# Kernel optimization log

Hardware: AMD Instinct MI355X
Metric: run time of the kernel (lower is better)

Reference implementation:

```python
import jax, jax.numpy as jnp
import numpy as np

N_NODES = 10000
W_DIM = 512
N_EDGES = 200000


def setup_inputs() -> dict:
    key = jax.random.key(0)
    k1, k2, k3 = jax.random.split(key, 3)
    z_drug = jax.random.normal(k1, (N_NODES, W_DIM), dtype=jnp.float32)
    # glorot-style init for the bilinear weight
    glorot_std = jnp.sqrt(2.0 / (W_DIM + W_DIM)).astype(jnp.float32)
    weight = jax.random.normal(k2, (W_DIM, W_DIM), dtype=jnp.float32) * glorot_std
    batch_edges = jax.random.randint(k3, (2, N_EDGES), 0, N_NODES, dtype=jnp.int64)
    return {"z_drug": z_drug, "weight": weight, "batch_edges": batch_edges}


def reference(z_drug, weight, batch_edges):
    # edge_type == 'drug_drug': both endpoints come from the drug table.
    row_embed = z_drug[batch_edges[0]]  # [E, d]
    col_embed = z_drug[batch_edges[1]]  # [E, d]
    # score_e = row_e @ W @ col_e  == diag((Z1 W) Z2^T) without the N x N blowup
    score = jnp.einsum('ed,df,ef->e', row_embed, weight, col_embed)
    return jax.nn.sigmoid(score)  # is_sigmoid=True default
```

## Files before the change

### kernel.cpp

```cpp
#include <hip/hip_runtime.h>
#include <math.h>

#define DIM     512
#define NNODES  10000
#define NEDGES  200000
#define MPAD    10048
#define NMB     157
#define NGRP    5
#define NB      (NGRP * NNODES)
#define SCAN_N  49
#define GEMM_GRID (NMB * 4)

#define HIST_BLK   50
#define SCAN_BASE  50
#define SCAT_BASE  99
#define SCAT_N     98
#define GEMM_BASE  197
#define FUSE_GRID  (GEMM_BASE + GEMM_GRID)

using floatx4 = __attribute__((ext_vector_type(4))) float;
using half8   = __attribute__((ext_vector_type(8))) _Float16;
using half2v  = __attribute__((ext_vector_type(2))) _Float16;

__device__ inline float dot2acc(half2v a, half2v b, float c) {
#if __has_builtin(__builtin_amdgcn_fdot2)
    return __builtin_amdgcn_fdot2(a, b, c, false);
#else
    return fmaf((float)a[0], (float)b[0], fmaf((float)a[1], (float)b[1], c));
#endif
}

__device__ inline int aload(const int* p) {
    return __hip_atomic_load(p, __ATOMIC_RELAXED, __HIP_MEMORY_SCOPE_AGENT);
}
__device__ inline void astore(int* p, int v) {
    __hip_atomic_store(p, v, __ATOMIC_RELAXED, __HIP_MEMORY_SCOPE_AGENT);
}
__device__ inline void waitflag(int* f, int target) {
    while (__hip_atomic_load(f, __ATOMIC_RELAXED, __HIP_MEMORY_SCOPE_AGENT) < target)
        __builtin_amdgcn_s_sleep(8);
    __atomic_signal_fence(__ATOMIC_ACQUIRE);
}
__device__ inline void signal(int* f) {
    __atomic_signal_fence(__ATOMIC_RELEASE);
    __hip_atomic_fetch_add(f, 1, __ATOMIC_RELAXED, __HIP_MEMORY_SCOPE_AGENT);
}

#define PREP_ZBLK 2512
__global__ __launch_bounds__(256) void prep(const float* __restrict__ Z,
                                            const float* __restrict__ W,
                                            _Float16* __restrict__ Zh16,
                                            _Float16* __restrict__ Wh16t,
                                            int* __restrict__ counts,
                                            int* __restrict__ flags) {
    const int b = blockIdx.x;
    const int t = threadIdx.x;

    if (b == 0 && t < 4) flags[t] = 0;

    if (b < 196) {
        int i = b * 256 + t;
        if (i < NB) counts[i] = 0;
    }

    if (b < PREP_ZBLK) {
        const int idx8 = (b * 256 + t) * 8;
        const int m = idx8 >> 9;
        float x[8];
        if (m < NNODES) {
            float4 v0 = *(const float4*)(Z + idx8);
            float4 v1 = *(const float4*)(Z + idx8 + 4);
            x[0]=v0.x; x[1]=v0.y; x[2]=v0.z; x[3]=v0.w;
            x[4]=v1.x; x[5]=v1.y; x[6]=v1.z; x[7]=v1.w;
        } else {
            #pragma unroll
            for (int j = 0; j < 8; ++j) x[j] = 0.f;
        }
        half8 h;
        #pragma unroll
        for (int j = 0; j < 8; ++j) h[j] = (_Float16)x[j];
        *(half8*)(Zh16 + idx8) = h;
    } else {
        __shared__ float tile[64][65];
        const int wb = b - PREP_ZBLK;
        const int kb = (wb >> 3) * 64;
        const int nb = (wb & 7) * 64;
        const int kk = t >> 2;
        const int ch = t & 3;

        const float* src = W + (size_t)(kb + kk) * DIM + nb + ch * 16;
        #pragma unroll
        for (int q = 0; q < 4; ++q) {
            float4 v = *(const float4*)(src + q * 4);
            tile[kk][ch * 16 + q * 4 + 0] = v.x;
            tile[kk][ch * 16 + q * 4 + 1] = v.y;
            tile[kk][ch * 16 + q * 4 + 2] = v.z;
            tile[kk][ch * 16 + q * 4 + 3] = v.w;
        }
        __syncthreads();

        const int nn = kk;
        half8 h0, h1;
        #pragma unroll
        for (int i = 0; i < 8; ++i) h0[i] = (_Float16)tile[ch * 16 + i][nn];
        #pragma unroll
        for (int i = 0; i < 8; ++i) h1[i] = (_Float16)tile[ch * 16 + 8 + i][nn];
        _Float16* d = Wh16t + (size_t)(nb + nn) * DIM + kb + ch * 16;
        *(half8*)(d)     = h0;
        *(half8*)(d + 8) = h1;
    }
}

__global__ __launch_bounds__(256, 3) void gemm_sort(
        const _Float16* __restrict__ Zh16,
        const _Float16* __restrict__ Wh16t,
        _Float16* __restrict__ ZWh,
        const int* __restrict__ eidx,
        int* __restrict__ counts,
        int* __restrict__ cursor,
        int* __restrict__ blksum,
        unsigned* __restrict__ keys,
        unsigned short* __restrict__ rows16,
        int* __restrict__ flags)
{
    __shared__ _Float16 Abuf[2][2 * 64 * 32];
    __shared__ _Float16 Bbuf[2][2 * 128 * 32];
    __shared__ int wsum[4];
    __shared__ int sbase;

    const int t   = threadIdx.x;
    const int bid = blockIdx.x;

    if (bid >= GEMM_BASE) {
        const int vb    = bid - GEMM_BASE;
        const int n_idx = vb & 3;
        const int m0    = (vb >> 2) * 64;
        const int n0    = n_idx * 128;

        const int l  = t & 63;
        const int w  = t >> 6;
        const int wn = w * 32;
        const int lm = l & 15;
        const int lq = l >> 4;
        const unsigned wbase = (unsigned)(t & 192);

        floatx4 acc[4][2] = {};

        auto stage = [&](int buf, int k0) {
            #pragma unroll
            for (int p = 0; p < 2; ++p) {
                const int s   = p * 256 + t;
                const int kk  = s >> 8;
                const int row = (s >> 2) & 63;
                const int ch  = s & 3;
                const _Float16* src = Zh16 + (size_t)(m0 + row) * DIM + k0 + kk * 32 + ch * 8;
                __builtin_amdgcn_global_load_lds(
                    (const __attribute__((address_space(1))) void*)src,
                    (__attribute__((address_space(3))) void*)&Abuf[buf][(p * 256 + wbase) * 8],
                    16, 0, 0);
            }
            #pragma unroll
            for (int p = 0; p < 4; ++p) {
                const int s   = p * 256 + t;
                const int kk  = s >> 9;
                const int row = (s >> 2) & 127;
                const int ch  = s & 3;
                const _Float16* src = Wh16t + (size_t)(n0 + row) * DIM + k0 + kk * 32 + ch * 8;
                __builtin_amdgcn_global_load_lds(
                    (const __attribute__((address_space(1))) void*)src,
                    (__attribute__((address_space(3))) void*)&Bbuf[buf][(p * 256 + wbase) * 8],
                    16, 0, 0);
            }
        };

        stage(0, 0);
        __syncthreads();

        for (int s = 0; s < 8; ++s) {
            const int buf = s & 1;
            if (s < 7) stage(buf ^ 1, (s + 1) * 64);

            #pragma unroll
            for (int kk = 0; kk < 2; ++kk) {
                half8 aF[4], bF[2];
                #pragma unroll
                for (int i = 0; i < 4; ++i)
                    aF[i] = *(const half8*)&Abuf[buf][kk * 2048 + (16 * i + lm) * 32 + lq * 8];
                #pragma unroll
                for (int j = 0; j < 2; ++j)
                    bF[j] = *(const half8*)&Bbuf[buf][kk * 4096 + (wn + 16 * j + lm) * 32 + lq * 8];

                #pragma unroll
                for (int i = 0; i < 4; ++i)
                    #pragma unroll
                    for (int j = 0; j < 2; ++j)
                        acc[i][j] = __builtin_amdgcn_mfma_f32_16x16x32_f16(aF[i], bF[j], acc[i][j], 0, 0, 0);
            }
            __syncthreads();
        }

        #pragma unroll
        for (int i = 0; i < 4; ++i)
            #pragma unroll
            for (int j = 0; j < 2; ++j)
                #pragma unroll
                for (int r = 0; r < 4; ++r) {
                    const int gm = m0 + 16 * i + lq * 4 + r;
                    const int gn = n0 + wn + 16 * j + lm;
                    if (gm < NNODES)
                        ZWh[(size_t)gm * DIM + gn] = (_Float16)acc[i][j][r];
                }
        return;
    }

    if (bid < HIST_BLK) {
        for (int e = bid * 256 + t; e < NEDGES; e += HIST_BLK * 256) {
            int r = eidx[e];
            int c = eidx[NEDGES + e];
            atomicAdd(&counts[(c >> 11) * NNODES + r], 1);
        }
        __syncthreads();
        if (t == 0) signal(&flags[0]);
        return;
    }

    if (bid < SCAT_BASE) {
        const int b = bid - SCAN_BASE;
        const int lane = t & 63;
        const int wv   = t >> 6;

        if (t == 0) waitflag(&flags[0], HIST_BLK);
        __syncthreads();

        const int base = b * 1024 + t * 4;
        int v0 = 0, v1 = 0, v2 = 0, v3 = 0;
        if (base + 3 < NB) {
            v0 = aload(counts + base);
            v1 = aload(counts + base + 1);
            v2 = aload(counts + base + 2);
            v3 = aload(counts + base + 3);
        } else {
            if (base     < NB) v0 = aload(counts + base);
            if (base + 1 < NB) v1 = aload(counts + base + 1);
            if (base + 2 < NB) v2 = aload(counts + base + 2);
        }
        const int ts = v0 + v1 + v2 + v3;
        int incl = ts;
        #pragma unroll
        for (int off = 1; off < 64; off <<= 1) {
            int u = __shfl_up(incl, off, 64);
            if (lane >= off) incl += u;
        }
        if (lane == 63) wsum[wv] = incl;
        __syncthreads();
        int wb = 0;
        #pragma unroll
        for (int k = 0; k < 4; ++k) if (k < wv) wb += wsum[k];
        const int ex   = wb + incl - ts;
        const int pre0 = ex;
        const int pre1 = ex + v0;
        const int pre2 = pre1 + v1;
        const int pre3 = pre2 + v2;
        if (t == 255) astore(blksum + b, wb + incl);
        __syncthreads();
        if (t == 0) { signal(&flags[1]); waitflag(&flags[1], SCAN_N); }
        __syncthreads();

        if (t < 64) {
            int v = (t < b) ? aload(blksum + t) : 0;
            #pragma unroll
            for (int off = 32; off > 0; off >>= 1)
                v += __shfl_xor(v, off, 64);
            if (t == 0) sbase = v;
        }
        __syncthreads();
        const int b0 = sbase;

        if (base + 3 < NB) {
            astore(cursor + base,     b0 + pre0);
            astore(cursor + base + 1, b0 + pre1);
            astore(cursor + base + 2, b0 + pre2);
            astore(cursor + base + 3, b0 + pre3);
        } else {
            if (base     < NB) astore(cursor + base,     b0 + pre0);
            if (base + 1 < NB) astore(cursor + base + 1, b0 + pre1);
            if (base + 2 < NB) astore(cursor + base + 2, b0 + pre2);
        }
        __syncthreads();
        if (t == 0) signal(&flags[2]);
        return;
    }

    {
        if (t == 0) waitflag(&flags[2], SCAN_N);
        __syncthreads();

        for (int e = (bid - SCAT_BASE) * 256 + t; e < NEDGES; e += SCAT_N * 256) {
            int r = eidx[e];
            int c = eidx[NEDGES + e];
            int pos = atomicAdd(&cursor[(c >> 11) * NNODES + r], 1);
            keys[pos]   = ((unsigned)c << 18) | (unsigned)e;
            rows16[pos] = (unsigned short)r;
        }
    }
}

__global__ __launch_bounds__(256) void edge_score_f(const _Float16* __restrict__ ZWh,
                                                    const _Float16* __restrict__ Zh,
                                                    const unsigned* __restrict__ keys,
                                                    const unsigned short* __restrict__ rows16,
                                                    float* __restrict__ out) {
    const int t    = threadIdx.x;
    const int wgid = blockIdx.x * 4 + (t >> 6);
    const int lane = t & 63;
    const int gq   = lane >> 4;
    const int sl   = lane & 15;

    const int ii = wgid * 4 + gq;
    const unsigned k = keys[ii];
    const int c = (int)(k >> 18);
    const int r = (int)rows16[ii];

    const _Float16* rp = ZWh + (size_t)r * DIM + sl * 32;
    const _Float16* cp = Zh  + (size_t)c * DIM + sl * 32;

    half8 ra0 = *(const half8*)(rp);
    half8 ra1 = *(const half8*)(rp + 8);
    half8 ra2 = *(const half8*)(rp + 16);
    half8 ra3 = *(const half8*)(rp + 24);
    half8 c0  = *(const half8*)(cp);
    half8 c1  = *(const half8*)(cp + 8);
    half8 c2  = *(const half8*)(cp + 16);
    half8 c3  = *(const half8*)(cp + 24);

    float s = 0.f;
    #pragma unroll
    for (int d = 0; d < 4; ++d) {
        s = dot2acc((half2v){ra0[2*d], ra0[2*d+1]}, (half2v){c0[2*d], c0[2*d+1]}, s);
        s = dot2acc((half2v){ra1[2*d], ra1[2*d+1]}, (half2v){c1[2*d], c1[2*d+1]}, s);
        s = dot2acc((half2v){ra2[2*d], ra2[2*d+1]}, (half2v){c2[2*d], c2[2*d+1]}, s);
        s = dot2acc((half2v){ra3[2*d], ra3[2*d+1]}, (half2v){c3[2*d], c3[2*d+1]}, s);
    }

    s += __shfl_xor(s, 1, 64);
    s += __shfl_xor(s, 2, 64);
    s += __shfl_xor(s, 4, 64);
    s += __shfl_xor(s, 8, 64);

    if (sl == 0)
        out[k & 0x3FFFFu] = 1.0f / (1.0f + expf(-s));
}

#define GTM 128
#define GTN 64
#define GTK 16
#define LDA 132
#define LDB 68

__global__ __launch_bounds__(256) void gemm_zw(const float* __restrict__ A,
                                               const float* __restrict__ B,
                                               float* __restrict__ C) {
    __shared__ float As[GTK * LDA];
    __shared__ float Bs[GTK * LDB];

    const int t  = threadIdx.x;
    const int m0 = blockIdx.x * GTM;
    const int n0 = blockIdx.y * GTN;
    const int tx = t & 15;
    const int ty = t >> 4;

    float acc[8][4] = {};

    for (int k0 = 0; k0 < DIM; k0 += GTK) {
        #pragma unroll
        for (int p = 0; p < 2; ++p) {
            int f  = t + p * 256;
            int mm = f >> 2;
            int kq = f & 3;
            int m  = m0 + mm;
            float4 v = make_float4(0.f, 0.f, 0.f, 0.f);
            if (m < NNODES)
                v = *(const float4*)(A + (size_t)m * DIM + k0 + kq * 4);
            As[(kq * 4 + 0) * LDA + mm] = v.x;
            As[(kq * 4 + 1) * LDA + mm] = v.y;
            As[(kq * 4 + 2) * LDA + mm] = v.z;
            As[(kq * 4 + 3) * LDA + mm] = v.w;
        }
        {
            int kb = t >> 4, n4 = t & 15;
            *(float4*)&Bs[kb * LDB + n4 * 4] =
                *(const float4*)(B + (size_t)(k0 + kb) * DIM + n0 + n4 * 4);
        }
        __syncthreads();

        #pragma unroll
        for (int kk = 0; kk < GTK; ++kk) {
            float4 a0 = *(const float4*)&As[kk * LDA + ty * 8];
            float4 a1 = *(const float4*)&As[kk * LDA + ty * 8 + 4];
            float4 b  = *(const float4*)&Bs[kk * LDB + tx * 4];
            float av[8] = {a0.x, a0.y, a0.z, a0.w, a1.x, a1.y, a1.z, a1.w};
            float bv[4] = {b.x, b.y, b.z, b.w};
            #pragma unroll
            for (int i = 0; i < 8; ++i)
                #pragma unroll
                for (int j = 0; j < 4; ++j)
                    acc[i][j] = fmaf(av[i], bv[j], acc[i][j]);
        }
        __syncthreads();
    }

    #pragma unroll
    for (int i = 0; i < 8; ++i) {
        int m = m0 + ty * 8 + i;
        if (m < NNODES)
            *(float4*)(C + (size_t)m * DIM + n0 + tx * 4) =
                make_float4(acc[i][0], acc[i][1], acc[i][2], acc[i][3]);
    }
}

__global__ __launch_bounds__(256) void edge_score(const float* __restrict__ ZW,
                                                  const float* __restrict__ Z,
                                                  const int* __restrict__ eidx,
                                                  float* __restrict__ out) {
    const int e    = blockIdx.x * 4 + (threadIdx.x >> 6);
    const int lane = threadIdx.x & 63;

    const int r = eidx[e];
    const int c = eidx[NEDGES + e];

    const float4* pr = (const float4*)(ZW + (size_t)r * DIM);
    const float4* pc = (const float4*)(Z  + (size_t)c * DIM);

    float4 a0 = pr[lane * 2 + 0];
    float4 a1 = pr[lane * 2 + 1];
    float4 b0 = pc[lane * 2 + 0];
    float4 b1 = pc[lane * 2 + 1];

    float s = a0.x * b0.x;
    s = fmaf(a0.y, b0.y, s);
    s = fmaf(a0.z, b0.z, s);
    s = fmaf(a0.w, b0.w, s);
    s = fmaf(a1.x, b1.x, s);
    s = fmaf(a1.y, b1.y, s);
    s = fmaf(a1.z, b1.z, s);
    s = fmaf(a1.w, b1.w, s);

    #pragma unroll
    for (int off = 32; off > 0; off >>= 1)
        s += __shfl_xor(s, off, 64);

    if (lane == 0)
        out[e] = 1.0f / (1.0f + expf(-s));
}

extern "C" void kernel_launch(void* const* d_in, const int* in_sizes, int n_in,
                              void* d_out, int out_size, void* d_ws, size_t ws_size,
                              hipStream_t stream) {
    const float* Z  = (const float*)d_in[0];
    const float* W  = (const float*)d_in[1];
    const int*   EI = (const int*)d_in[2];
    float* out = (float*)d_out;

    char* p = (char*)d_ws;
    _Float16* ZWh   = (_Float16*)p;  p += (size_t)MPAD * DIM * 2;
    _Float16* Zh16  = (_Float16*)p;  p += (size_t)MPAD * DIM * 2;
    _Float16* Wh16t = (_Float16*)p;  p += (size_t)DIM * DIM * 2;
    int* counts  = (int*)p;          p += (size_t)NB * 4;
    int* cursor  = (int*)p;          p += (size_t)NB * 4;
    int* blksum  = (int*)p;          p += (size_t)SCAN_N * 4;
    unsigned* keys = (unsigned*)p;   p += (size_t)NEDGES * 4;
    unsigned short* rows16 = (unsigned short*)p; p += (size_t)NEDGES * 2;
    int* flags = (int*)p;            p += 4 * 4;
    const size_t need_full = (size_t)(p - (char*)d_ws);

    if (ws_size >= need_full) {
        prep<<<PREP_ZBLK + 64, 256, 0, stream>>>(Z, W, Zh16, Wh16t, counts, flags);
        gemm_sort<<<FUSE_GRID, 256, 0, stream>>>(Zh16, Wh16t, ZWh, EI, counts,
                                                 cursor, blksum, keys, rows16, flags);
        edge_score_f<<<NEDGES / 16, 256, 0, stream>>>(ZWh, Zh16, keys, rows16, out);
    } else {
        float* ZW = (float*)d_ws;
        dim3 g1((NNODES + GTM - 1) / GTM, DIM / GTN);
        gemm_zw<<<g1, 256, 0, stream>>>(Z, W, ZW);
        edge_score<<<NEDGES / 4, 256, 0, stream>>>(ZW, Z, EI, out);
    }
}
```

Baseline: 138.5 us.

## Load GEMM MFMA fragments directly from global memory, dropping LDS staging

The GEMM blocks of the fused kernel stop staging A and B tiles through double-buffered LDS with global_load_lds and barriers. Each wave now reads its MFMA operand fragments directly from global memory in a fully unrolled K loop. This frees the shared-memory buffers and raises the launch-bounds occupancy hint from 3 to 4 blocks. The cost is that A fragments are reloaded by all four waves and there is no explicit prefetch, so the loop relies on L1/L2 hits and compiler scheduling to hide load latency.

```diff
diff --git a/kernel.cpp b/kernel.cpp
--- a/kernel.cpp
+++ b/kernel.cpp
@@ -111,7 +111,7 @@
     }
 }
 
-__global__ __launch_bounds__(256, 3) void gemm_sort(
+__global__ __launch_bounds__(256, 4) void gemm_sort(
         const _Float16* __restrict__ Zh16,
         const _Float16* __restrict__ Wh16t,
         _Float16* __restrict__ ZWh,
@@ -123,8 +123,6 @@
         unsigned short* __restrict__ rows16,
         int* __restrict__ flags)
 {
-    __shared__ _Float16 Abuf[2][2 * 64 * 32];
-    __shared__ _Float16 Bbuf[2][2 * 128 * 32];
     __shared__ int wsum[4];
     __shared__ int sbase;
 
@@ -132,71 +130,41 @@
     const int bid = blockIdx.x;
 
     if (bid >= GEMM_BASE) {
-        const int vb    = bid - GEMM_BASE;
-        const int n_idx = vb & 3;
-        const int m0    = (vb >> 2) * 64;
-        const int n0    = n_idx * 128;
+        const int vb  = bid - GEMM_BASE;
+        const int m0  = (vb >> 2) * 64;
+        const int n0w = (vb & 3) * 128 + (t >> 6) * 32;
 
         const int l  = t & 63;
-        const int w  = t >> 6;
-        const int wn = w * 32;
         const int lm = l & 15;
         const int lq = l >> 4;
-        const unsigned wbase = (unsigned)(t & 192);
+
+        const _Float16* pa0 = Zh16 + (size_t)(m0 + lm) * DIM + lq * 8;
+        const _Float16* pa1 = pa0 + (size_t)16 * DIM;
+        const _Float16* pa2 = pa0 + (size_t)32 * DIM;
+        const _Float16* pa3 = pa0 + (size_t)48 * DIM;
+        const _Float16* pb0 = Wh16t + (size_t)(n0w + lm) * DIM + lq * 8;
+        const _Float16* pb1 = pb0 + (size_t)16 * DIM;
 
         floatx4 acc[4][2] = {};
 
-        auto stage = [&](int buf, int k0) {
-            #pragma unroll
-            for (int p = 0; p < 2; ++p) {
-                const int s   = p * 256 + t;
-                const int kk  = s >> 8;
-                const int row = (s >> 2) & 63;
-                const int ch  = s & 3;
-                const _Float16* src = Zh16 + (size_t)(m0 + row) * DIM + k0 + kk * 32 + ch * 8;
-                __builtin_amdgcn_global_load_lds(
-                    (const __attribute__((address_space(1))) void*)src,
-                    (__attribute__((address_space(3))) void*)&Abuf[buf][(p * 256 + wbase) * 8],
-                    16, 0, 0);
-            }
-            #pragma unroll
-            for (int p = 0; p < 4; ++p) {
-                const int s   = p * 256 + t;
-                const int kk  = s >> 9;
-                const int row = (s >> 2) & 127;
-                const int ch  = s & 3;
-                const _Float16* src = Wh16t + (size_t)(n0 + row) * DIM + k0 + kk * 32 + ch * 8;
-                __builtin_amdgcn_global_load_lds(
-                    (const __attribute__((address_space(1))) void*)src,
-                    (__attribute__((address_space(3))) void*)&Bbuf[buf][(p * 256 + wbase) * 8],
-                    16, 0, 0);
-            }
-        };
-
-        stage(0, 0);
-        __syncthreads();
-
-        for (int s = 0; s < 8; ++s) {
-            const int buf = s & 1;
-            if (s < 7) stage(buf ^ 1, (s + 1) * 64);
-
-            #pragma unroll
-            for (int kk = 0; kk < 2; ++kk) {
-                half8 aF[4], bF[2];
-                #pragma unroll
-                for (int i = 0; i < 4; ++i)
-                    aF[i] = *(const half8*)&Abuf[buf][kk * 2048 + (16 * i + lm) * 32 + lq * 8];
-                #pragma unroll
-                for (int j = 0; j < 2; ++j)
-                    bF[j] = *(const half8*)&Bbuf[buf][kk * 4096 + (wn + 16 * j + lm) * 32 + lq * 8];
-
-                #pragma unroll
-                for (int i = 0; i < 4; ++i)
-                    #pragma unroll
-                    for (int j = 0; j < 2; ++j)
-                        acc[i][j] = __builtin_amdgcn_mfma_f32_16x16x32_f16(aF[i], bF[j], acc[i][j], 0, 0, 0);
-            }
-            __syncthreads();
+        #pragma unroll
+        for (int s = 0; s < 16; ++s) {
+            const int off = s * 32;
+            half8 a0 = *(const half8*)(pa0 + off);
+            half8 a1 = *(const half8*)(pa1 + off);
+            half8 a2 = *(const half8*)(pa2 + off);
+            half8 a3 = *(const half8*)(pa3 + off);
+            half8 b0 = *(const half8*)(pb0 + off);
+            half8 b1 = *(const half8*)(pb1 + off);
+
+            acc[0][0] = __builtin_amdgcn_mfma_f32_16x16x32_f16(a0, b0, acc[0][0], 0, 0, 0);
+            acc[0][1] = __builtin_amdgcn_mfma_f32_16x16x32_f16(a0, b1, acc[0][1], 0, 0, 0);
+            acc[1][0] = __builtin_amdgcn_mfma_f32_16x16x32_f16(a1, b0, acc[1][0], 0, 0, 0);
+            acc[1][1] = __builtin_amdgcn_mfma_f32_16x16x32_f16(a1, b1, acc[1][1], 0, 0, 0);
+            acc[2][0] = __builtin_amdgcn_mfma_f32_16x16x32_f16(a2, b0, acc[2][0], 0, 0, 0);
+            acc[2][1] = __builtin_amdgcn_mfma_f32_16x16x32_f16(a2, b1, acc[2][1], 0, 0, 0);
+            acc[3][0] = __builtin_amdgcn_mfma_f32_16x16x32_f16(a3, b0, acc[3][0], 0, 0, 0);
+            acc[3][1] = __builtin_amdgcn_mfma_f32_16x16x32_f16(a3, b1, acc[3][1], 0, 0, 0);
         }
 
         #pragma unroll
@@ -206,7 +174,7 @@
                 #pragma unroll
                 for (int r = 0; r < 4; ++r) {
                     const int gm = m0 + 16 * i + lq * 4 + r;
-                    const int gn = n0 + wn + 16 * j + lm;
+                    const int gn = n0w + 16 * j + lm;
                     if (gm < NNODES)
                         ZWh[(size_t)gm * DIM + gn] = (_Float16)acc[i][j][r];
                 }
```

Measured after the change: 149.2 us. 1.08x slower.
